# Kernel optimization log

Measured on AMD Instinct MI355X. Metric: run time of the kernel, lower is better.

The kernel has to match this reference:

```python
import jax, jax.numpy as jnp
import numpy as np

N_NETS = 76  # 29 h2o + 13 o3 + 9 co2 + 3 n2o + 9 ch4 + 13 u
N_CH = 29
N_KE = [29, 13, 9, 3, 9, 13]
# which composition column each of the 76 nets is scaled by
GAS_OF_NET = np.repeat(np.arange(6), N_KE)
# which output channel each of the 76 tau terms is added into (hardcoded table in subcall)
CHAN_OF_NET = np.concatenate([
    np.arange(29),                                            # h2o[i] -> channel i
    np.array([0, 1, 2, 17, 18, 19, 20, 21, 22, 25, 26, 27, 28]),  # o3
    np.array([0, 1, 2, 5, 6, 9, 10, 13, 14]),                 # co2
    np.array([0, 1, 2]),                                      # n2o
    np.array([0, 1, 2, 3, 4, 7, 8, 11, 12]),                  # ch4
    np.array([0, 1, 2, 15, 16, 17, 18, 19, 20, 21, 22, 27, 28]),  # u
])


def setup_inputs() -> dict:
    key = jax.random.key(0)
    ks = jax.random.split(key, 16)
    B, D_IN, H = 262144, 2, 4
    t_p = jax.random.normal(ks[0], (B, D_IN), dtype=jnp.float32)
    composition = jax.random.uniform(ks[1], (B, 8), dtype=jnp.float32)
    null_lw = jnp.zeros((B, 1), dtype=jnp.float32)
    null_iw = jnp.zeros((B, 1), dtype=jnp.float32)
    # stacked params of the 76 tiny DenseFFNs (hidden [4,4], elu; out 1, softplus)
    W1 = jax.random.normal(ks[2], (N_NETS, D_IN, H), dtype=jnp.float32) * 0.5
    b1 = jax.random.normal(ks[3], (N_NETS, H), dtype=jnp.float32) * 0.05
    W2 = jax.random.normal(ks[4], (N_NETS, H, H), dtype=jnp.float32) * 0.5
    b2 = jax.random.normal(ks[5], (N_NETS, H), dtype=jnp.float32) * 0.05
    W3 = jax.random.uniform(ks[6], (N_NETS, H, 1), minval=-1.0, maxval=1.0, dtype=jnp.float32)
    b3 = jnp.zeros((N_NETS, 1), dtype=jnp.float32)
    # per-channel lw / iw Dense(1) layers (input dim 1)
    W_lw = jax.random.normal(ks[7], (N_CH,), dtype=jnp.float32) * 0.5
    b_lw = jax.random.uniform(ks[8], (N_CH,), minval=0.0, maxval=1.0, dtype=jnp.float32)
    W_iw = jax.random.normal(ks[9], (N_CH,), dtype=jnp.float32) * 0.5
    b_iw = jax.random.uniform(ks[10], (N_CH,), minval=0.0, maxval=1.0, dtype=jnp.float32)
    return {"t_p": t_p, "composition": composition, "null_lw": null_lw, "null_iw": null_iw,
            "W1": W1, "b1": b1, "W2": W2, "b2": b2, "W3": W3, "b3": b3,
            "W_lw": W_lw, "b_lw": b_lw, "W_iw": W_iw, "b_iw": b_iw}


def reference(t_p, composition, null_lw, null_iw, W1, b1, W2, b2, W3, b3, W_lw, b_lw, W_iw, b_iw):
    # all 76 tiny MLPs batched as one einsum chain: [n_nets, B, h]
    h = jax.nn.elu(jnp.einsum('bi,nio->nbo', t_p, W1) + b1[:, None, :])
    h = jax.nn.elu(jnp.einsum('nbi,nio->nbo', h, W2) + b2[:, None, :])
    ke = jax.nn.softplus(jnp.einsum('nbi,nio->nbo', h, W3) + b3[:, None, :])[..., 0]  # [76, B]
    # scale each net's output by its gas concentration, then scatter-add into 29 channels
    tau = ke * composition[:, GAS_OF_NET].T                                  # [76, B]
    tau_gases = jax.ops.segment_sum(tau, jnp.asarray(CHAN_OF_NET), num_segments=N_CH)  # [29, B]
    tau_gases = jnp.transpose(tau_gases)[:, :, None]                          # [B, 29, 1]
    # lw / iw: softplus(null * w_c + b_c) * composition[:, 6 or 7]
    tau_lw = (jax.nn.softplus(null_lw * W_lw[None, :] + b_lw[None, :]) * composition[:, 6:7])[:, :, None]
    tau_iw = (jax.nn.softplus(null_iw * W_iw[None, :] + b_iw[None, :]) * composition[:, 7:8])[:, :, None]
    return (tau_gases, tau_lw, tau_iw)
```

## Files before the change

### kernel.cpp

```cpp
#include <hip/hip_runtime.h>
#include <cstdint>

#define BLOCK 256
#define ROWS 128
#define NREC 40

typedef float v2f __attribute__((ext_vector_type(2)));

__device__ __forceinline__ float exp2s(float x) { return __builtin_amdgcn_exp2f(x); }
__device__ __forceinline__ float log2s(float x) { return __builtin_amdgcn_logf(x); }
__device__ __forceinline__ v2f exp22(v2f x) { return (v2f){exp2s(x.x), exp2s(x.y)}; }
__device__ __forceinline__ v2f fma2(v2f a, v2f b, v2f c) { return __builtin_elementwise_fma(a, b, c); }
__device__ __forceinline__ v2f max2(v2f a, v2f b) { return __builtin_elementwise_max(a, b); }
__device__ __forceinline__ v2f min2(v2f a, v2f b) { return __builtin_elementwise_min(a, b); }
__device__ __forceinline__ v2f abs2(v2f a) { return __builtin_elementwise_abs(a); }
__device__ __forceinline__ v2f splat(float s) { return (v2f){s, s}; }

#define LN2 0.6931471805599453f
#define L2E 1.4426950408889634f

constexpr int GAS_[76] = {
    0,0,0,0,0,0,0,0,0,0,0,0,0,0,0,0,0,0,0,0,0,0,0,0,0,0,0,0,0,
    1,1,1,1,1,1,1,1,1,1,1,1,1,
    2,2,2,2,2,2,2,2,2,
    3,3,3,
    4,4,4,4,4,4,4,4,4,
    5,5,5,5,5,5,5,5,5,5,5,5,5};
constexpr int CHAN_[76] = {
    0,1,2,3,4,5,6,7,8,9,10,11,12,13,14,15,16,17,18,19,20,21,22,23,24,25,26,27,28,
    0,1,2,17,18,19,20,21,22,25,26,27,28,
    0,1,2,5,6,9,10,13,14,
    0,1,2,
    0,1,2,3,4,7,8,11,12,
    0,1,2,15,16,17,18,19,20,21,22,27,28};

__global__ void __launch_bounds__(128)
prep_kernel(const float* __restrict__ W1, const float* __restrict__ b1,
            const float* __restrict__ W2, const float* __restrict__ b2,
            const float* __restrict__ W3, const float* __restrict__ b3,
            const float* __restrict__ W_lw, const float* __restrict__ b_lw,
            const float* __restrict__ W_iw, const float* __restrict__ b_iw,
            float* __restrict__ rec)
{
    const int n = threadIdx.x;
    if (n < 76) {
        float* r = rec + n * NREC;
        #pragma unroll
        for (int k = 0; k < 8; ++k) r[k] = W1[n * 8 + k] * L2E;
        #pragma unroll
        for (int o = 0; o < 4; ++o) r[8 + o] = b1[n * 4 + o] * L2E;
        #pragma unroll
        for (int k = 0; k < 16; ++k) r[12 + k] = W2[n * 16 + k] * L2E;
        #pragma unroll
        for (int o = 0; o < 4; ++o) {
            float s = 0.0f;
            #pragma unroll
            for (int i = 0; i < 4; ++i) s += W2[n * 16 + i * 4 + o];
            r[28 + o] = (b2[n * 4 + o] - s) * L2E;
        }
        float s3 = 0.0f;
        #pragma unroll
        for (int i = 0; i < 4; ++i) { r[32 + i] = W3[n * 4 + i] * L2E; s3 += W3[n * 4 + i]; }
        r[36] = (b3[n] - s3) * L2E;
        r[37] = 0.0f; r[38] = 0.0f; r[39] = 0.0f;
    } else if (n < 76 + 29) {
        const int ch = n - 76;
        float* t = rec + 76 * NREC + ch * 4;
        t[0] = W_lw[ch] * L2E;
        t[1] = b_lw[ch] * L2E;
        t[2] = W_iw[ch] * L2E;
        t[3] = b_iw[ch] * L2E;
    }
}

__device__ __forceinline__ v2f elu_h2(v2f as) {
    return max2(fma2(as, splat(LN2), splat(1.0f)), exp22(min2(as, splat(0.0f))));
}

template<int NS, int NE>
__device__ __forceinline__ void run_nets2(
    const float* __restrict__ rec, v2f tpx, v2f tpy,
    const v2f* cgl2 , v2f* tau)
{
    #pragma unroll
    for (int n = NS; n < NE; ++n) {
        const float* __restrict__ R = rec + n * NREC;
        v2f H1[4];
        #pragma unroll
        for (int o = 0; o < 4; ++o)
            H1[o] = elu_h2(fma2(tpx, splat(R[o]), fma2(tpy, splat(R[4 + o]), splat(R[8 + o]))));
        v2f H2[4];
        #pragma unroll
        for (int o = 0; o < 4; ++o) {
            v2f a = splat(R[28 + o]);
            #pragma unroll
            for (int i = 0; i < 4; ++i)
                a = fma2(H1[i], splat(R[12 + i * 4 + o]), a);
            H2[o] = elu_h2(a);
        }
        v2f a3 = splat(R[36]);
        #pragma unroll
        for (int i = 0; i < 4; ++i)
            a3 = fma2(H2[i], splat(R[32 + i]), a3);
        const v2f e = exp22(-abs2(a3));
        const v2f sp = max2(a3, splat(0.0f)) +
                       (v2f){log2s(1.0f + e.x), log2s(1.0f + e.y)};
        tau[CHAN_[n]] = fma2(sp, cgl2[GAS_[n]], tau[CHAN_[n]]);
    }
}

template<bool EXACT>
__global__ void __launch_bounds__(BLOCK)
od_kernel(const float* __restrict__ t_p,
          const float* __restrict__ comp,
          const float* __restrict__ null_lw,
          const float* __restrict__ null_iw,
          const float* __restrict__ rec,
          float* __restrict__ out, int B)
{
    __shared__ float stage[2][ROWS * 29];

    const int wave = threadIdx.x >> 6;
    const int lane = threadIdx.x & 63;
    const int base = blockIdx.x * ROWS;
    int r0 = base + lane;
    int r1 = base + 64 + lane;
    if (!EXACT) { r0 = r0 < B ? r0 : B - 1; r1 = r1 < B ? r1 : B - 1; }

    const float2 ta = *reinterpret_cast<const float2*>(t_p + (size_t)r0 * 2);
    const float2 tb = *reinterpret_cast<const float2*>(t_p + (size_t)r1 * 2);
    const v2f tpx = {ta.x, tb.x};
    const v2f tpy = {ta.y, tb.y};

    const float4 ca0 = *reinterpret_cast<const float4*>(comp + (size_t)r0 * 8);
    const float2 cb0 = *reinterpret_cast<const float2*>(comp + (size_t)r0 * 8 + 4);
    const float4 ca1 = *reinterpret_cast<const float4*>(comp + (size_t)r1 * 8);
    const float2 cb1 = *reinterpret_cast<const float2*>(comp + (size_t)r1 * 8 + 4);
    const v2f cgl2[6] = {
        {ca0.x * LN2, ca1.x * LN2}, {ca0.y * LN2, ca1.y * LN2},
        {ca0.z * LN2, ca1.z * LN2}, {ca0.w * LN2, ca1.w * LN2},
        {cb0.x * LN2, cb1.x * LN2}, {cb0.y * LN2, cb1.y * LN2}};

    v2f tau[29];
    #pragma unroll
    for (int i = 0; i < 29; ++i) tau[i] = splat(0.0f);

    switch (wave) {
        case 0: run_nets2< 0, 19>(rec, tpx, tpy, cgl2, tau); break;
        case 1: run_nets2<19, 38>(rec, tpx, tpy, cgl2, tau); break;
        case 2: run_nets2<38, 57>(rec, tpx, tpy, cgl2, tau); break;
        default: run_nets2<57, 76>(rec, tpx, tpy, cgl2, tau); break;
    }

    if (wave < 2) {
        #pragma unroll
        for (int i = 0; i < 29; ++i) {
            stage[wave][lane * 29 + i] = tau[i].x;
            stage[wave][(lane + 64) * 29 + i] = tau[i].y;
        }
    }
    __syncthreads();
    if (wave >= 2) {
        float* p = stage[wave - 2];
        #pragma unroll
        for (int i = 0; i < 29; ++i) {
            p[lane * 29 + i] += tau[i].x;
            p[(lane + 64) * 29 + i] += tau[i].y;
        }
    }
    __syncthreads();

    const size_t obase = (size_t)base * 29;
    const size_t BN = (size_t)B * 29;
    const int lim = EXACT ? (ROWS * 29)
                          : (((B - base < ROWS) ? (B - base) : ROWS) * 29);
    const float* __restrict__ recL = rec + 76 * NREC;

    for (int idx = threadIdx.x; idx < lim; idx += BLOCK) {
        out[obase + idx] = stage[0][idx] + stage[1][idx];
        const int r  = idx / 29;
        const int ch = idx - r * 29;
        const int grow = base + r;
        const float nl = null_lw[grow];
        const float ni = null_iw[grow];
        const float c6 = comp[(size_t)grow * 8 + 6] * LN2;
        const float c7 = comp[(size_t)grow * 8 + 7] * LN2;
        const float4 L = *reinterpret_cast<const float4*>(recL + ch * 4);
        const float alw = fmaf(nl, L.x, L.y);
        const float aiw = fmaf(ni, L.z, L.w);
        out[BN + obase + idx] =
            (fmaxf(alw, 0.0f) + log2s(1.0f + exp2s(-fabsf(alw)))) * c6;
        out[2 * BN + obase + idx] =
            (fmaxf(aiw, 0.0f) + log2s(1.0f + exp2s(-fabsf(aiw)))) * c7;
    }
}

extern "C" void kernel_launch(void* const* d_in, const int* in_sizes, int n_in,
                              void* d_out, int out_size, void* d_ws, size_t ws_size,
                              hipStream_t stream) {
    const float* t_p     = (const float*)d_in[0];
    const float* comp    = (const float*)d_in[1];
    const float* null_lw = (const float*)d_in[2];
    const float* null_iw = (const float*)d_in[3];
    const float* W1      = (const float*)d_in[4];
    const float* b1      = (const float*)d_in[5];
    const float* W2      = (const float*)d_in[6];
    const float* b2      = (const float*)d_in[7];
    const float* W3      = (const float*)d_in[8];
    const float* b3      = (const float*)d_in[9];
    const float* W_lw    = (const float*)d_in[10];
    const float* b_lw    = (const float*)d_in[11];
    const float* W_iw    = (const float*)d_in[12];
    const float* b_iw    = (const float*)d_in[13];
    float* out = (float*)d_out;
    float* rec = (float*)d_ws;

    const int B = in_sizes[0] / 2;

    prep_kernel<<<1, 128, 0, stream>>>(W1, b1, W2, b2, W3, b3,
                                       W_lw, b_lw, W_iw, b_iw, rec);

    const int blocks = (B + ROWS - 1) / ROWS;
    if (B % ROWS == 0)
        od_kernel<true><<<blocks, BLOCK, 0, stream>>>(t_p, comp, null_lw, null_iw,
                                                      rec, out, B);
    else
        od_kernel<false><<<blocks, BLOCK, 0, stream>>>(t_p, comp, null_lw, null_iw,
                                                       rec, out, B);
}
```

Measured before the change: 60.97 us.

## Pack net pairs in packed-float lanes instead of row pairs per thread

Rather than processing two batch rows per thread with packed math, each thread now handles one row and evaluates two nets at once in the v2f lanes. The weight records are interleaved in pairs of nets so each packed FMA takes a vector weight operand instead of a broadcast scalar. ROWS is halved to 64, which doubles the block count. The intent is to cut the per-net weight-load cost and register pressure, at the price of scalar tau accumulation and half as much batch work per thread.

```diff
diff --git a/kernel.cpp b/kernel.cpp
--- a/kernel.cpp
+++ b/kernel.cpp
@@ -2,8 +2,8 @@
 #include <cstdint>
 
 #define BLOCK 256
-#define ROWS 128
-#define NREC 40
+#define ROWS 64
+#define NRECP 76
 
 typedef float v2f __attribute__((ext_vector_type(2)));
 
@@ -42,30 +42,48 @@
             const float* __restrict__ W_iw, const float* __restrict__ b_iw,
             float* __restrict__ rec)
 {
-    const int n = threadIdx.x;
-    if (n < 76) {
-        float* r = rec + n * NREC;
-        #pragma unroll
-        for (int k = 0; k < 8; ++k) r[k] = W1[n * 8 + k] * L2E;
-        #pragma unroll
-        for (int o = 0; o < 4; ++o) r[8 + o] = b1[n * 4 + o] * L2E;
-        #pragma unroll
-        for (int k = 0; k < 16; ++k) r[12 + k] = W2[n * 16 + k] * L2E;
+    const int p = threadIdx.x;
+    if (p < 38) {
+        const int nA = 2 * p, nB = 2 * p + 1;
+        float* r = rec + p * NRECP;
+        #pragma unroll
+        for (int k = 0; k < 8; ++k) {
+            r[2 * k]     = W1[nA * 8 + k] * L2E;
+            r[2 * k + 1] = W1[nB * 8 + k] * L2E;
+        }
         #pragma unroll
         for (int o = 0; o < 4; ++o) {
-            float s = 0.0f;
+            r[16 + 2 * o]     = b1[nA * 4 + o] * L2E;
+            r[16 + 2 * o + 1] = b1[nB * 4 + o] * L2E;
+        }
+        #pragma unroll
+        for (int k = 0; k < 16; ++k) {
+            r[24 + 2 * k]     = W2[nA * 16 + k] * L2E;
+            r[24 + 2 * k + 1] = W2[nB * 16 + k] * L2E;
+        }
+        #pragma unroll
+        for (int o = 0; o < 4; ++o) {
+            float sA = 0.0f, sB = 0.0f;
             #pragma unroll
-            for (int i = 0; i < 4; ++i) s += W2[n * 16 + i * 4 + o];
-            r[28 + o] = (b2[n * 4 + o] - s) * L2E;
-        }
-        float s3 = 0.0f;
-        #pragma unroll
-        for (int i = 0; i < 4; ++i) { r[32 + i] = W3[n * 4 + i] * L2E; s3 += W3[n * 4 + i]; }
-        r[36] = (b3[n] - s3) * L2E;
-        r[37] = 0.0f; r[38] = 0.0f; r[39] = 0.0f;
-    } else if (n < 76 + 29) {
-        const int ch = n - 76;
-        float* t = rec + 76 * NREC + ch * 4;
+            for (int i = 0; i < 4; ++i) {
+                sA += W2[nA * 16 + i * 4 + o];
+                sB += W2[nB * 16 + i * 4 + o];
+            }
+            r[56 + 2 * o]     = (b2[nA * 4 + o] - sA) * L2E;
+            r[56 + 2 * o + 1] = (b2[nB * 4 + o] - sB) * L2E;
+        }
+        float s3A = 0.0f, s3B = 0.0f;
+        #pragma unroll
+        for (int i = 0; i < 4; ++i) {
+            r[64 + 2 * i]     = W3[nA * 4 + i] * L2E;  s3A += W3[nA * 4 + i];
+            r[64 + 2 * i + 1] = W3[nB * 4 + i] * L2E;  s3B += W3[nB * 4 + i];
+        }
+        r[72] = (b3[nA] - s3A) * L2E;
+        r[73] = (b3[nB] - s3B) * L2E;
+        r[74] = 0.0f; r[75] = 0.0f;
+    } else if (p < 38 + 29) {
+        const int ch = p - 38;
+        float* t = rec + 38 * NRECP + ch * 4;
         t[0] = W_lw[ch] * L2E;
         t[1] = b_lw[ch] * L2E;
         t[2] = W_iw[ch] * L2E;
@@ -77,35 +95,38 @@
     return max2(fma2(as, splat(LN2), splat(1.0f)), exp22(min2(as, splat(0.0f))));
 }
 
-template<int NS, int NE>
-__device__ __forceinline__ void run_nets2(
-    const float* __restrict__ rec, v2f tpx, v2f tpy,
-    const v2f* cgl2 , v2f* tau)
+template<int PS, int PE>
+__device__ __forceinline__ void run_pairs(
+    const float* __restrict__ rec, float tpx, float tpy,
+    const float* cgl2 , float* tau)
 {
+    const v2f tpx2 = splat(tpx);
+    const v2f tpy2 = splat(tpy);
     #pragma unroll
-    for (int n = NS; n < NE; ++n) {
-        const float* __restrict__ R = rec + n * NREC;
+    for (int p = PS; p < PE; ++p) {
+        const v2f* __restrict__ RP = (const v2f*)(rec + p * NRECP);
         v2f H1[4];
         #pragma unroll
         for (int o = 0; o < 4; ++o)
-            H1[o] = elu_h2(fma2(tpx, splat(R[o]), fma2(tpy, splat(R[4 + o]), splat(R[8 + o]))));
+            H1[o] = elu_h2(fma2(tpx2, RP[o], fma2(tpy2, RP[4 + o], RP[8 + o])));
         v2f H2[4];
         #pragma unroll
         for (int o = 0; o < 4; ++o) {
-            v2f a = splat(R[28 + o]);
+            v2f a = RP[28 + o];
             #pragma unroll
             for (int i = 0; i < 4; ++i)
-                a = fma2(H1[i], splat(R[12 + i * 4 + o]), a);
+                a = fma2(H1[i], RP[12 + i * 4 + o], a);
             H2[o] = elu_h2(a);
         }
-        v2f a3 = splat(R[36]);
+        v2f a3 = RP[36];
         #pragma unroll
         for (int i = 0; i < 4; ++i)
-            a3 = fma2(H2[i], splat(R[32 + i]), a3);
+            a3 = fma2(H2[i], RP[32 + i], a3);
         const v2f e = exp22(-abs2(a3));
         const v2f sp = max2(a3, splat(0.0f)) +
                        (v2f){log2s(1.0f + e.x), log2s(1.0f + e.y)};
-        tau[CHAN_[n]] = fma2(sp, cgl2[GAS_[n]], tau[CHAN_[n]]);
+        tau[CHAN_[2 * p]]     = fmaf(sp.x, cgl2[GAS_[2 * p]],     tau[CHAN_[2 * p]]);
+        tau[CHAN_[2 * p + 1]] = fmaf(sp.y, cgl2[GAS_[2 * p + 1]], tau[CHAN_[2 * p + 1]]);
     }
 }
 
@@ -123,50 +144,35 @@
     const int wave = threadIdx.x >> 6;
     const int lane = threadIdx.x & 63;
     const int base = blockIdx.x * ROWS;
-    int r0 = base + lane;
-    int r1 = base + 64 + lane;
-    if (!EXACT) { r0 = r0 < B ? r0 : B - 1; r1 = r1 < B ? r1 : B - 1; }
-
-    const float2 ta = *reinterpret_cast<const float2*>(t_p + (size_t)r0 * 2);
-    const float2 tb = *reinterpret_cast<const float2*>(t_p + (size_t)r1 * 2);
-    const v2f tpx = {ta.x, tb.x};
-    const v2f tpy = {ta.y, tb.y};
-
-    const float4 ca0 = *reinterpret_cast<const float4*>(comp + (size_t)r0 * 8);
-    const float2 cb0 = *reinterpret_cast<const float2*>(comp + (size_t)r0 * 8 + 4);
-    const float4 ca1 = *reinterpret_cast<const float4*>(comp + (size_t)r1 * 8);
-    const float2 cb1 = *reinterpret_cast<const float2*>(comp + (size_t)r1 * 8 + 4);
-    const v2f cgl2[6] = {
-        {ca0.x * LN2, ca1.x * LN2}, {ca0.y * LN2, ca1.y * LN2},
-        {ca0.z * LN2, ca1.z * LN2}, {ca0.w * LN2, ca1.w * LN2},
-        {cb0.x * LN2, cb1.x * LN2}, {cb0.y * LN2, cb1.y * LN2}};
-
-    v2f tau[29];
+    const int row  = EXACT ? (base + lane)
+                           : ((base + lane < B) ? (base + lane) : (B - 1));
+
+    const float2 tp = *reinterpret_cast<const float2*>(t_p + (size_t)row * 2);
+    const float4 ca = *reinterpret_cast<const float4*>(comp + (size_t)row * 8);
+    const float2 cb = *reinterpret_cast<const float2*>(comp + (size_t)row * 8 + 4);
+    const float cgl2[6] = {ca.x * LN2, ca.y * LN2, ca.z * LN2,
+                           ca.w * LN2, cb.x * LN2, cb.y * LN2};
+
+    float tau[29];
     #pragma unroll
-    for (int i = 0; i < 29; ++i) tau[i] = splat(0.0f);
+    for (int i = 0; i < 29; ++i) tau[i] = 0.0f;
 
     switch (wave) {
-        case 0: run_nets2< 0, 19>(rec, tpx, tpy, cgl2, tau); break;
-        case 1: run_nets2<19, 38>(rec, tpx, tpy, cgl2, tau); break;
-        case 2: run_nets2<38, 57>(rec, tpx, tpy, cgl2, tau); break;
-        default: run_nets2<57, 76>(rec, tpx, tpy, cgl2, tau); break;
+        case 0: run_pairs< 0, 10>(rec, tp.x, tp.y, cgl2, tau); break;
+        case 1: run_pairs<10, 20>(rec, tp.x, tp.y, cgl2, tau); break;
+        case 2: run_pairs<20, 29>(rec, tp.x, tp.y, cgl2, tau); break;
+        default: run_pairs<29, 38>(rec, tp.x, tp.y, cgl2, tau); break;
     }
 
     if (wave < 2) {
         #pragma unroll
-        for (int i = 0; i < 29; ++i) {
-            stage[wave][lane * 29 + i] = tau[i].x;
-            stage[wave][(lane + 64) * 29 + i] = tau[i].y;
-        }
+        for (int i = 0; i < 29; ++i) stage[wave][lane * 29 + i] = tau[i];
     }
     __syncthreads();
     if (wave >= 2) {
         float* p = stage[wave - 2];
         #pragma unroll
-        for (int i = 0; i < 29; ++i) {
-            p[lane * 29 + i] += tau[i].x;
-            p[(lane + 64) * 29 + i] += tau[i].y;
-        }
+        for (int i = 0; i < 29; ++i) p[lane * 29 + i] += tau[i];
     }
     __syncthreads();
 
@@ -174,7 +180,7 @@
     const size_t BN = (size_t)B * 29;
     const int lim = EXACT ? (ROWS * 29)
                           : (((B - base < ROWS) ? (B - base) : ROWS) * 29);
-    const float* __restrict__ recL = rec + 76 * NREC;
+    const float* __restrict__ recL = rec + 38 * NRECP;
 
     for (int idx = threadIdx.x; idx < lim; idx += BLOCK) {
         out[obase + idx] = stage[0][idx] + stage[1][idx];
```

Result: faster. 59.70 us (-2.1%).

## Replace per-wave register tau arrays with shared-memory atomic accumulation

Applied to the files above, without the earlier changes.

Each wave used to hold a 29-entry register accumulator, with net indices fixed at compile time through a switch. Now one loop is shared by all waves, using a wave-uniform offset into the parameter records, and the channel and gas indices are stored in the records themselves. Per-net contributions go into a shared-memory tau array through LDS atomicAdd, which removes the two-stage staging reduction and is meant to cut register pressure and code size. In exchange it adds runtime-indexed LDS reads for the composition values and an LDS atomic per net per row, plus an extra barrier.

```diff
diff --git a/kernel.cpp b/kernel.cpp
--- a/kernel.cpp
+++ b/kernel.cpp
@@ -2,7 +2,7 @@
 #include <cstdint>
 
 #define BLOCK 256
-#define ROWS 128
+#define RPB 128
 #define NREC 40
 
 typedef float v2f __attribute__((ext_vector_type(2)));
@@ -62,7 +62,9 @@
         #pragma unroll
         for (int i = 0; i < 4; ++i) { r[32 + i] = W3[n * 4 + i] * L2E; s3 += W3[n * 4 + i]; }
         r[36] = (b3[n] - s3) * L2E;
-        r[37] = 0.0f; r[38] = 0.0f; r[39] = 0.0f;
+        r[37] = __uint_as_float((unsigned)CHAN_[n]);
+        r[38] = __uint_as_float((unsigned)GAS_[n]);
+        r[39] = 0.0f;
     } else if (n < 76 + 29) {
         const int ch = n - 76;
         float* t = rec + 76 * NREC + ch * 4;
@@ -75,38 +77,6 @@
 
 __device__ __forceinline__ v2f elu_h2(v2f as) {
     return max2(fma2(as, splat(LN2), splat(1.0f)), exp22(min2(as, splat(0.0f))));
-}
-
-template<int NS, int NE>
-__device__ __forceinline__ void run_nets2(
-    const float* __restrict__ rec, v2f tpx, v2f tpy,
-    const v2f* cgl2 , v2f* tau)
-{
-    #pragma unroll
-    for (int n = NS; n < NE; ++n) {
-        const float* __restrict__ R = rec + n * NREC;
-        v2f H1[4];
-        #pragma unroll
-        for (int o = 0; o < 4; ++o)
-            H1[o] = elu_h2(fma2(tpx, splat(R[o]), fma2(tpy, splat(R[4 + o]), splat(R[8 + o]))));
-        v2f H2[4];
-        #pragma unroll
-        for (int o = 0; o < 4; ++o) {
-            v2f a = splat(R[28 + o]);
-            #pragma unroll
-            for (int i = 0; i < 4; ++i)
-                a = fma2(H1[i], splat(R[12 + i * 4 + o]), a);
-            H2[o] = elu_h2(a);
-        }
-        v2f a3 = splat(R[36]);
-        #pragma unroll
-        for (int i = 0; i < 4; ++i)
-            a3 = fma2(H2[i], splat(R[32 + i]), a3);
-        const v2f e = exp22(-abs2(a3));
-        const v2f sp = max2(a3, splat(0.0f)) +
-                       (v2f){log2s(1.0f + e.x), log2s(1.0f + e.y)};
-        tau[CHAN_[n]] = fma2(sp, cgl2[GAS_[n]], tau[CHAN_[n]]);
-    }
 }
 
 template<bool EXACT>
@@ -118,66 +88,87 @@
           const float* __restrict__ rec,
           float* __restrict__ out, int B)
 {
-    __shared__ float stage[2][ROWS * 29];
-
-    const int wave = threadIdx.x >> 6;
-    const int lane = threadIdx.x & 63;
-    const int base = blockIdx.x * ROWS;
+    __shared__ float tauL[RPB * 29];
+    __shared__ float cgL[RPB * 9];
+
+    const int tid  = threadIdx.x;
+    const int wave = tid >> 6;
+    const int lane = tid & 63;
+    const int base = blockIdx.x * RPB;
     int r0 = base + lane;
     int r1 = base + 64 + lane;
-    if (!EXACT) { r0 = r0 < B ? r0 : B - 1; r1 = r1 < B ? r1 : B - 1; }
+    bool v0 = true, v1 = true;
+    if (!EXACT) {
+        v0 = r0 < B; v1 = r1 < B;
+        r0 = v0 ? r0 : B - 1;
+        r1 = v1 ? r1 : B - 1;
+    }
 
     const float2 ta = *reinterpret_cast<const float2*>(t_p + (size_t)r0 * 2);
     const float2 tb = *reinterpret_cast<const float2*>(t_p + (size_t)r1 * 2);
     const v2f tpx = {ta.x, tb.x};
     const v2f tpy = {ta.y, tb.y};
 
-    const float4 ca0 = *reinterpret_cast<const float4*>(comp + (size_t)r0 * 8);
-    const float2 cb0 = *reinterpret_cast<const float2*>(comp + (size_t)r0 * 8 + 4);
-    const float4 ca1 = *reinterpret_cast<const float4*>(comp + (size_t)r1 * 8);
-    const float2 cb1 = *reinterpret_cast<const float2*>(comp + (size_t)r1 * 8 + 4);
-    const v2f cgl2[6] = {
-        {ca0.x * LN2, ca1.x * LN2}, {ca0.y * LN2, ca1.y * LN2},
-        {ca0.z * LN2, ca1.z * LN2}, {ca0.w * LN2, ca1.w * LN2},
-        {cb0.x * LN2, cb1.x * LN2}, {cb0.y * LN2, cb1.y * LN2}};
-
-    v2f tau[29];
+    for (int i = tid; i < RPB * 29; i += BLOCK) tauL[i] = 0.0f;
+    if (tid < RPB) {
+        int grow = base + tid;
+        if (!EXACT) grow = grow < B ? grow : B - 1;
+        const float4 ca = *reinterpret_cast<const float4*>(comp + (size_t)grow * 8);
+        const float2 cb = *reinterpret_cast<const float2*>(comp + (size_t)grow * 8 + 4);
+        float* c = cgL + tid * 9;
+        c[0] = ca.x * LN2; c[1] = ca.y * LN2; c[2] = ca.z * LN2;
+        c[3] = ca.w * LN2; c[4] = cb.x * LN2; c[5] = cb.y * LN2;
+    }
+    __syncthreads();
+
+    const int woff = __builtin_amdgcn_readfirstlane(wave * 19);
+    const float* __restrict__ Rb = rec + (size_t)woff * NREC;
+
     #pragma unroll
-    for (int i = 0; i < 29; ++i) tau[i] = splat(0.0f);
-
-    switch (wave) {
-        case 0: run_nets2< 0, 19>(rec, tpx, tpy, cgl2, tau); break;
-        case 1: run_nets2<19, 38>(rec, tpx, tpy, cgl2, tau); break;
-        case 2: run_nets2<38, 57>(rec, tpx, tpy, cgl2, tau); break;
-        default: run_nets2<57, 76>(rec, tpx, tpy, cgl2, tau); break;
-    }
-
-    if (wave < 2) {
-        #pragma unroll
-        for (int i = 0; i < 29; ++i) {
-            stage[wave][lane * 29 + i] = tau[i].x;
-            stage[wave][(lane + 64) * 29 + i] = tau[i].y;
+    for (int j = 0; j < 19; ++j) {
+        const float* __restrict__ R = Rb + j * NREC;
+        v2f H1[4];
+        #pragma unroll
+        for (int o = 0; o < 4; ++o)
+            H1[o] = elu_h2(fma2(tpx, splat(R[o]), fma2(tpy, splat(R[4 + o]), splat(R[8 + o]))));
+        v2f H2[4];
+        #pragma unroll
+        for (int o = 0; o < 4; ++o) {
+            v2f a = splat(R[28 + o]);
+            #pragma unroll
+            for (int i = 0; i < 4; ++i)
+                a = fma2(H1[i], splat(R[12 + i * 4 + o]), a);
+            H2[o] = elu_h2(a);
         }
+        v2f a3 = splat(R[36]);
+        #pragma unroll
+        for (int i = 0; i < 4; ++i)
+            a3 = fma2(H2[i], splat(R[32 + i]), a3);
+        const v2f e = exp22(-abs2(a3));
+        const v2f sp = max2(a3, splat(0.0f)) +
+                       (v2f){log2s(1.0f + e.x), log2s(1.0f + e.y)};
+
+        const unsigned chan = __float_as_uint(R[37]);
+        const unsigned gas  = __float_as_uint(R[38]);
+        const float cg0 = cgL[lane * 9 + gas];
+        const float cg1 = cgL[(lane + 64) * 9 + gas];
+        if (EXACT || v0) atomicAdd(&tauL[lane * 29 + chan],        sp.x * cg0);
+        if (EXACT || v1) atomicAdd(&tauL[(lane + 64) * 29 + chan], sp.y * cg1);
     }
     __syncthreads();
-    if (wave >= 2) {
-        float* p = stage[wave - 2];
-        #pragma unroll
-        for (int i = 0; i < 29; ++i) {
-            p[lane * 29 + i] += tau[i].x;
-            p[(lane + 64) * 29 + i] += tau[i].y;
-        }
-    }
-    __syncthreads();
-
+
+    const size_t BN = (size_t)B * 29;
     const size_t obase = (size_t)base * 29;
-    const size_t BN = (size_t)B * 29;
-    const int lim = EXACT ? (ROWS * 29)
-                          : (((B - base < ROWS) ? (B - base) : ROWS) * 29);
     const float* __restrict__ recL = rec + 76 * NREC;
-
-    for (int idx = threadIdx.x; idx < lim; idx += BLOCK) {
-        out[obase + idx] = stage[0][idx] + stage[1][idx];
+    int lim = RPB * 29;
+    if (!EXACT) {
+        int rrem = B - base;
+        rrem = rrem < 0 ? 0 : (rrem > RPB ? RPB : rrem);
+        lim = rrem * 29;
+    }
+
+    for (int idx = tid; idx < lim; idx += BLOCK) {
+        out[obase + idx] = tauL[idx];
         const int r  = idx / 29;
         const int ch = idx - r * 29;
         const int grow = base + r;
@@ -220,8 +211,8 @@
     prep_kernel<<<1, 128, 0, stream>>>(W1, b1, W2, b2, W3, b3,
                                        W_lw, b_lw, W_iw, b_iw, rec);
 
-    const int blocks = (B + ROWS - 1) / ROWS;
-    if (B % ROWS == 0)
+    const int blocks = (B + RPB - 1) / RPB;
+    if (B % RPB == 0)
         od_kernel<true><<<blocks, BLOCK, 0, stream>>>(t_p, comp, null_lw, null_iw,
                                                       rec, out, B);
     else
```

Measured after the change: 119.4 us. 95.8% more time.
